# Kernel optimization log

Measured on AMD Instinct MI355X. Metric: run time of the kernel, lower is better.

Reference implementation:

```python
import jax, jax.numpy as jnp
import numpy as np

N = 100000   # nodes
E = 1600000  # edges
F_IN = 256   # nfeat
H = 64       # hidden_sizes
C = 40       # nclass


def gcn_norm(edge_index, edge_weight, num_nodes):
    # Add self-loops with weight 1 (PyG gcn_norm default fill_value=1.0)
    loop = jnp.arange(num_nodes)
    row = jnp.concatenate([edge_index[0], loop])
    col = jnp.concatenate([edge_index[1], loop])
    w = jnp.concatenate([edge_weight, jnp.ones((num_nodes,), edge_weight.dtype)])
    # Symmetric normalization: D^-1/2 A D^-1/2 (degree computed at target, per PyG)
    deg = jax.ops.segment_sum(w, col, num_segments=num_nodes)
    deg_inv_sqrt = jnp.where(deg > 0, jax.lax.rsqrt(deg), 0.0)
    norm = deg_inv_sqrt[row] * w * deg_inv_sqrt[col]
    return row, col, norm


def gcn_conv(x, W, b, row, col, norm, num_nodes):
    # Linear transform first (shrinks feature dim before irregular traffic)
    x = x @ W                                    # [N, out]
    msgs = norm[:, None] * x[row]                # gather + scale: [E+N, out]
    out = jax.ops.segment_sum(msgs, col, num_segments=num_nodes)  # scatter-add
    return out + b


def setup_inputs() -> dict:
    key = jax.random.key(0)
    k = jax.random.split(key, 7)
    x = jax.random.normal(k[0], (N, F_IN), dtype=jnp.float32)
    edge_index = jax.random.randint(k[1], (2, E), 0, N, dtype=jnp.int64)
    edge_attr = jax.random.uniform(k[2], (E,), dtype=jnp.float32)
    W1 = jax.random.normal(k[3], (F_IN, H), dtype=jnp.float32) * (1.0 / np.sqrt(F_IN))
    b1 = jnp.zeros((H,), jnp.float32)
    W2 = jax.random.normal(k[4], (H, C), dtype=jnp.float32) * (1.0 / np.sqrt(H))
    b2 = jnp.zeros((C,), jnp.float32)
    return {"x": x, "edge_index": edge_index, "edge_attr": edge_attr,
            "W1": W1, "b1": b1, "W2": W2, "b2": b2}


def reference(x, edge_index, edge_attr, W1, b1, W2, b2):
    row, col, norm = gcn_norm(edge_index, edge_attr, N)
    h = jax.nn.relu(gcn_conv(x, W1, b1, row, col, norm, N))
    # F.dropout with training=False is identity (eval mode)
    final = gcn_conv(h, W2, b2, row, col, norm, N)
    return final, jax.nn.log_softmax(final, axis=1)
```

## Files before the change

### kernel.cpp

```cpp
#include <hip/hip_runtime.h>
#include <hip/hip_bf16.h>
#include <math.h>

#define NN 100000
#define EE 1600000
#define FIN 256
#define HID 64
#define NC 40
#define NB 196
#define BCAP 10240
#define CHUNK 2048
#define NBKB ((EE + CHUNK - 1) / CHUNK)

typedef unsigned long long ull;
typedef __attribute__((ext_vector_type(8))) short short8;
typedef __attribute__((ext_vector_type(4))) float f32x4;

__device__ __forceinline__ unsigned short f2bf_rne(float f) {
    unsigned u = __float_as_uint(f);
    u += 0x7FFFu + ((u >> 16) & 1u);
    return (unsigned short)(u >> 16);
}
__device__ __forceinline__ float bf2f(unsigned short b) {
    return __uint_as_float((unsigned)b << 16);
}

__global__ __launch_bounds__(256) void bucket_kernel(const int* __restrict__ row,
                                                     const int* __restrict__ col,
                                                     const float* __restrict__ w,
                                                     int* __restrict__ bucket_cnt,
                                                     int2* __restrict__ staging) {
    __shared__ int2 spay[CHUNK];
    __shared__ int2 sorted[CHUNK];
    __shared__ unsigned char sb[CHUNK];
    __shared__ unsigned char sbk[CHUNK];
    __shared__ int lcnt[NB], lofs[NB], lstart[NB];
    __shared__ int sscan[256];
    const int tid = threadIdx.x;
    const int e0 = blockIdx.x * CHUNK;
    const int nE = min(CHUNK, EE - e0);
    for (int i = tid; i < nE; i += 256) {
        int e = e0 + i;
        int c = col[e];
        sb[i] = (unsigned char)(c >> 9);
        spay[i] = make_int2(((c & 511) << 17) | row[e], __float_as_int(w[e]));
    }
    for (int i = tid; i < NB; i += 256) lcnt[i] = 0;
    __syncthreads();
    for (int i = tid; i < nE; i += 256) atomicAdd(&lcnt[sb[i]], 1);
    __syncthreads();
    int v = (tid < NB) ? lcnt[tid] : 0;
    sscan[tid] = v;
    __syncthreads();
    for (int off = 1; off < 256; off <<= 1) {
        int u = (tid >= off) ? sscan[tid - off] : 0;
        __syncthreads();
        sscan[tid] += u;
        __syncthreads();
    }
    if (tid < NB) {
        lofs[tid] = sscan[tid] - v;
        lstart[tid] = v ? atomicAdd(&bucket_cnt[tid], v) : 0;
        lcnt[tid] = 0;
    }
    __syncthreads();
    for (int i = tid; i < nE; i += 256) {
        int b = sb[i];
        int p = lofs[b] + atomicAdd(&lcnt[b], 1);
        sorted[p] = spay[i];
        sbk[p] = (unsigned char)b;
    }
    __syncthreads();
    for (int p = tid; p < nE; p += 256) {
        int b = sbk[p];
        int slot = lstart[b] + (p - lofs[b]);
        if (slot < BCAP) staging[(size_t)b * BCAP + slot] = sorted[p];
    }
}

__global__ __launch_bounds__(256) void bscan_w1cvt_kernel(int* __restrict__ bucket_cnt,
                                                          int* __restrict__ bucket_base,
                                                          const float* __restrict__ W1,
                                                          unsigned short* __restrict__ w1hi,
                                                          unsigned short* __restrict__ w1lo) {
    if (blockIdx.x == 0) {
        __shared__ int sd[256];
        int t = threadIdx.x;
        int v = (t < NB) ? min(bucket_cnt[t], BCAP) : 0;
        sd[t] = v;
        __syncthreads();
        for (int off = 1; off < 256; off <<= 1) {
            int u = (t >= off) ? sd[t - off] : 0;
            __syncthreads();
            sd[t] += u;
            __syncthreads();
        }
        if (t < NB) { bucket_base[t] = sd[t] - v; bucket_cnt[t] = v; }
    } else {
        int b = blockIdx.x - 1;
        for (int i = threadIdx.x; i < 4096; i += 256) {
            int e = b * 4096 + i;
            int c = e >> 8, k = e & 255;
            float v = W1[(size_t)k * HID + c];
            unsigned short h = f2bf_rne(v);
            w1hi[e] = h;
            w1lo[e] = f2bf_rne(v - bf2f(h));
        }
    }
}

__global__ __launch_bounds__(512) void build_count_kernel(const int2* __restrict__ staging,
                                                          const int* __restrict__ bucket_cnt,
                                                          const int* __restrict__ bucket_base,
                                                          int* __restrict__ basev,
                                                          int* __restrict__ endv,
                                                          float* __restrict__ dis) {
    __shared__ int dcnt[512];
    __shared__ float dsum[512];
    __shared__ int sscan[512];
    const int t = threadIdx.x;
    const int b = blockIdx.x;
    const int nE = bucket_cnt[b];
    const int ebase = bucket_base[b];
    const int2* st = staging + (size_t)b * BCAP;
    dcnt[t] = 0; dsum[t] = 0.f;
    __syncthreads();
    for (int i = t; i < nE; i += 512) {
        int2 p = st[i];
        int d = p.x >> 17;
        atomicAdd(&dcnt[d], 1);
        atomicAdd(&dsum[d], __int_as_float(p.y));
    }
    __syncthreads();
    int c = dcnt[t];
    sscan[t] = c;
    __syncthreads();
    for (int off = 1; off < 512; off <<= 1) {
        int u = (t >= off) ? sscan[t - off] : 0;
        __syncthreads();
        sscan[t] += u;
        __syncthreads();
    }
    int gb = ebase + sscan[t] - c;
    int gd = b * 512 + t;
    if (gd < NN) {
        basev[gd] = gb;
        endv[gd] = gb + c;
        dis[gd] = rsqrtf(dsum[t] + 1.0f);
    }
}

__global__ __launch_bounds__(512) void build_place_kernel(const int2* __restrict__ staging,
                                                          const int* __restrict__ bucket_cnt,
                                                          const int* __restrict__ basev,
                                                          const float* __restrict__ dis,
                                                          int2* __restrict__ eme) {
    __shared__ int dcur[512];
    __shared__ float sdis[512];
    const int t = threadIdx.x;
    const int b = blockIdx.x;
    const int nE = bucket_cnt[b];
    const int2* st = staging + (size_t)b * BCAP;
    const int gd = b * 512 + t;
    dcur[t] = (gd < NN) ? basev[gd] : 0;
    sdis[t] = (gd < NN) ? dis[gd] : 0.f;
    __syncthreads();
    for (int i = t; i < nE; i += 512) {
        int2 p = st[i];
        int d = p.x >> 17;
        int src = p.x & 0x1FFFF;
        int pos = atomicAdd(&dcur[d], 1);
        float wn = __int_as_float(p.y) * dis[src] * sdis[d];
        eme[pos] = make_int2(src, __float_as_int(wn));
    }
}

__global__ __launch_bounds__(256) void gemm1_mfma_kernel(const float* __restrict__ x,
                                                         const unsigned short* __restrict__ w1hi,
                                                         const unsigned short* __restrict__ w1lo,
                                                         __hip_bfloat16* __restrict__ xw) {
    const int tid = threadIdx.x;
    const int wid = tid >> 6;
    const int l   = tid & 63;
    const int r   = l & 15;
    const int kg  = l >> 4;
    const int rb0 = blockIdx.x * 128 + wid * 32;

    f32x4 acc[2][4];
#pragma unroll
    for (int i = 0; i < 2; i++)
#pragma unroll
        for (int j = 0; j < 4; j++) acc[i][j] = (f32x4){0.f, 0.f, 0.f, 0.f};

    int row0 = rb0 + r;
    int row1 = rb0 + 16 + r;
    int row0c = row0 < NN ? row0 : NN - 1;
    int row1c = row1 < NN ? row1 : NN - 1;
    const float* a0p = x + (size_t)row0c * FIN + kg * 8;
    const float* a1p = x + (size_t)row1c * FIN + kg * 8;

#pragma unroll
    for (int ks = 0; ks < 8; ks++) {
        short8 bhi[4], blo[4];
#pragma unroll
        for (int ct = 0; ct < 4; ct++) {
            size_t off = (size_t)(ct * 16 + r) * FIN + ks * 32 + kg * 8;
            bhi[ct] = *(const short8*)(w1hi + off);
            blo[ct] = *(const short8*)(w1lo + off);
        }
        float4 af0a = *(const float4*)(a0p + ks * 32);
        float4 af0b = *(const float4*)(a0p + ks * 32 + 4);
        float4 af1a = *(const float4*)(a1p + ks * 32);
        float4 af1b = *(const float4*)(a1p + ks * 32 + 4);
        float a0v[8] = {af0a.x, af0a.y, af0a.z, af0a.w, af0b.x, af0b.y, af0b.z, af0b.w};
        float a1v[8] = {af1a.x, af1a.y, af1a.z, af1a.w, af1b.x, af1b.y, af1b.z, af1b.w};
        short8 ahi0, alo0, ahi1, alo1;
#pragma unroll
        for (int j = 0; j < 8; j++) {
            unsigned short h0 = f2bf_rne(a0v[j]);
            ahi0[j] = (short)h0;
            alo0[j] = (short)f2bf_rne(a0v[j] - bf2f(h0));
            unsigned short h1 = f2bf_rne(a1v[j]);
            ahi1[j] = (short)h1;
            alo1[j] = (short)f2bf_rne(a1v[j] - bf2f(h1));
        }
#pragma unroll
        for (int ct = 0; ct < 4; ct++) {
            acc[0][ct] = __builtin_amdgcn_mfma_f32_16x16x32_bf16(ahi0, bhi[ct], acc[0][ct], 0, 0, 0);
            acc[0][ct] = __builtin_amdgcn_mfma_f32_16x16x32_bf16(ahi0, blo[ct], acc[0][ct], 0, 0, 0);
            acc[0][ct] = __builtin_amdgcn_mfma_f32_16x16x32_bf16(alo0, bhi[ct], acc[0][ct], 0, 0, 0);
            acc[1][ct] = __builtin_amdgcn_mfma_f32_16x16x32_bf16(ahi1, bhi[ct], acc[1][ct], 0, 0, 0);
            acc[1][ct] = __builtin_amdgcn_mfma_f32_16x16x32_bf16(ahi1, blo[ct], acc[1][ct], 0, 0, 0);
            acc[1][ct] = __builtin_amdgcn_mfma_f32_16x16x32_bf16(alo1, bhi[ct], acc[1][ct], 0, 0, 0);
        }
    }
#pragma unroll
    for (int rt = 0; rt < 2; rt++) {
#pragma unroll
        for (int i = 0; i < 4; i++) {
            int grow = rb0 + rt * 16 + kg * 4 + i;
            if (grow < NN) {
                unsigned short* dst = (unsigned short*)xw + (size_t)grow * HID + r;
#pragma unroll
                for (int ct = 0; ct < 4; ct++)
                    dst[ct * 16] = f2bf_rne(acc[rt][ct][i]);
            }
        }
    }
}

__global__ __launch_bounds__(256) void gather1_kernel(const int* __restrict__ basev,
                                                      const int* __restrict__ endv,
                                                      const ull* __restrict__ eme,
                                                      const unsigned* __restrict__ xw32,
                                                      const float* __restrict__ dis,
                                                      const float* __restrict__ b,
                                                      float* __restrict__ h) {
    int n = blockIdx.x * 4 + (threadIdx.x >> 6);
    if (n >= NN) return;
    int lane = threadIdx.x & 63;
    int half = lane >> 5;
    int fl = lane & 31;
    int s = basev[n], t = endv[n];
    int deg = t - s;
    float acc0 = 0.f, acc1 = 0.f;
    int nbt = (deg + 15) >> 4;
    for (int bi = 0; bi < nbt; bi++) {
        int p0 = s + bi * 16 + half;
        ull q[8];
#pragma unroll
        for (int j = 0; j < 8; j++) {
            int idx = p0 + 2 * j;
            int c = idx < t ? idx : (t - 1);
            q[j] = __builtin_nontemporal_load(&eme[c]);
        }
        unsigned u[8];
        float wv[8];
#pragma unroll
        for (int j = 0; j < 8; j++) {
            unsigned src = (unsigned)q[j] & 0x1FFFFu;
            u[j] = xw32[(src << 5) | fl];
            wv[j] = (p0 + 2 * j < t) ? __int_as_float((int)(q[j] >> 32)) : 0.f;
        }
#pragma unroll
        for (int j = 0; j < 8; j++) {
            acc0 += wv[j] * __uint_as_float(u[j] << 16);
            acc1 += wv[j] * __uint_as_float(u[j] & 0xFFFF0000u);
        }
    }
    acc0 += __shfl_xor(acc0, 32);
    acc1 += __shfl_xor(acc1, 32);
    float d = dis[n];
    unsigned un = xw32[((unsigned)n << 5) | fl];
    float2 bv = *(const float2*)(b + 2 * fl);
    float v0 = acc0 + d * d * __uint_as_float(un << 16) + bv.x;
    float v1 = acc1 + d * d * __uint_as_float(un & 0xFFFF0000u) + bv.y;
    if (lane < 32) {
        *(float2*)(h + (size_t)n * HID + 2 * fl) = make_float2(fmaxf(v0, 0.f), fmaxf(v1, 0.f));
    }
}

__global__ __launch_bounds__(256) void gemm2_kernel(const float* __restrict__ h,
                                                    const float* __restrict__ W,
                                                    __hip_bfloat16* __restrict__ hw) {
    __shared__ float hs[64][65];
    __shared__ float Ws[HID * NC];
    const int tid = threadIdx.x;
    const int base = blockIdx.x * 64;
    for (int v = tid; v < 1024; v += 256) {
        int r = v >> 4, q = v & 15;
        int gr = base + r;
        float4 hv = make_float4(0.f, 0.f, 0.f, 0.f);
        if (gr < NN) hv = *(const float4*)(h + (size_t)gr * HID + q * 4);
        hs[r][q * 4 + 0] = hv.x; hs[r][q * 4 + 1] = hv.y;
        hs[r][q * 4 + 2] = hv.z; hs[r][q * 4 + 3] = hv.w;
    }
    for (int v = tid; v < HID * NC; v += 256) Ws[v] = W[v];
    __syncthreads();
    const int tx = tid & 7;
    const int ty = tid >> 3;
    float acc[2][5] = {};
#pragma unroll 8
    for (int k = 0; k < HID; k++) {
        float h0 = hs[ty * 2 + 0][k];
        float h1 = hs[ty * 2 + 1][k];
        const float* wr = &Ws[k * NC + tx * 5];
        float w0 = wr[0], w1 = wr[1], w2 = wr[2], w3 = wr[3], w4 = wr[4];
        acc[0][0] += h0 * w0; acc[0][1] += h0 * w1; acc[0][2] += h0 * w2;
        acc[0][3] += h0 * w3; acc[0][4] += h0 * w4;
        acc[1][0] += h1 * w0; acc[1][1] += h1 * w1; acc[1][2] += h1 * w2;
        acc[1][3] += h1 * w3; acc[1][4] += h1 * w4;
    }
#pragma unroll
    for (int i = 0; i < 2; i++) {
        int gr = base + ty * 2 + i;
        if (gr < NN) {
#pragma unroll
            for (int c = 0; c < 5; c++)
                hw[(size_t)gr * 64 + tx * 5 + c] = __float2bfloat16(acc[i][c]);
        }
    }
}

__global__ __launch_bounds__(256) void gather2_kernel(const int* __restrict__ basev,
                                                      const int* __restrict__ endv,
                                                      const ull* __restrict__ eme,
                                                      const unsigned* __restrict__ hw32,
                                                      const float* __restrict__ dis,
                                                      const float* __restrict__ b,
                                                      float* __restrict__ out) {
    int n = blockIdx.x * 4 + (threadIdx.x >> 6);
    if (n >= NN) return;
    int lane = threadIdx.x & 63;
    int half = lane >> 5;
    int fl = lane & 31;
    bool act = fl < 20;
    int s = basev[n], t = endv[n];
    int deg = t - s;
    float acc0 = 0.f, acc1 = 0.f;
    int nbt = (deg + 15) >> 4;
    for (int bi = 0; bi < nbt; bi++) {
        int p0 = s + bi * 16 + half;
        ull q[8];
#pragma unroll
        for (int j = 0; j < 8; j++) {
            int idx = p0 + 2 * j;
            int c = idx < t ? idx : (t - 1);
            q[j] = __builtin_nontemporal_load(&eme[c]);
        }
        unsigned u[8];
        float wv[8];
#pragma unroll
        for (int j = 0; j < 8; j++) {
            unsigned src = (unsigned)q[j] & 0x1FFFFu;
            u[j] = hw32[(src << 5) | fl];
            wv[j] = (p0 + 2 * j < t) ? __int_as_float((int)(q[j] >> 32)) : 0.f;
        }
#pragma unroll
        for (int j = 0; j < 8; j++) {
            acc0 += wv[j] * __uint_as_float(u[j] << 16);
            acc1 += wv[j] * __uint_as_float(u[j] & 0xFFFF0000u);
        }
    }
    acc0 += __shfl_xor(acc0, 32);
    acc1 += __shfl_xor(acc1, 32);
    float v0 = 0.f, v1 = 0.f, m = -INFINITY;
    if (act) {
        float d = dis[n];
        unsigned un = hw32[((unsigned)n << 5) | fl];
        float2 bv = *(const float2*)(b + 2 * fl);
        v0 = acc0 + d * d * __uint_as_float(un << 16) + bv.x;
        v1 = acc1 + d * d * __uint_as_float(un & 0xFFFF0000u) + bv.y;
        m = fmaxf(v0, v1);
    }
#pragma unroll
    for (int off = 16; off; off >>= 1) m = fmaxf(m, __shfl_xor(m, off));
    float e0 = act ? expf(v0 - m) : 0.f;
    float e1 = act ? expf(v1 - m) : 0.f;
    float sum = e0 + e1;
#pragma unroll
    for (int off = 16; off; off >>= 1) sum += __shfl_xor(sum, off);
    float lse = m + logf(sum);
    if (act && lane < 32) {
        size_t idx = (size_t)n * NC + 2 * fl;
        *(float2*)(out + idx) = make_float2(v0, v1);
        *(float2*)(out + (size_t)NN * NC + idx) = make_float2(v0 - lse, v1 - lse);
    }
}

extern "C" void kernel_launch(void* const* d_in, const int* in_sizes, int n_in,
                              void* d_out, int out_size, void* d_ws, size_t ws_size,
                              hipStream_t stream) {
    const float* x    = (const float*)d_in[0];
    const int*   eidx = (const int*)d_in[1];
    const float* ew   = (const float*)d_in[2];
    const float* W1   = (const float*)d_in[3];
    const float* b1   = (const float*)d_in[4];
    const float* W2   = (const float*)d_in[5];
    const float* b2   = (const float*)d_in[6];
    float* out = (float*)d_out;

    const int* row = eidx;
    const int* col = eidx + EE;

    char* ws = (char*)d_ws;
    int*   bucket_cnt  = (int*)ws;               ws += 256 * 4;
    int*   bucket_base = (int*)ws;               ws += 256 * 4;
    float* dis    = (float*)ws;                  ws += NN * 4;
    int*   basev  = (int*)ws;                    ws += NN * 4;
    int*   endv   = (int*)ws;                    ws += NN * 4;
    int2*  eme    = (int2*)ws;                   ws += (size_t)EE * 8;
    __hip_bfloat16* xw = (__hip_bfloat16*)ws;    ws += (size_t)NN * HID * 2;
    char* unionp = ws;                           ws += (size_t)NN * HID * 4;
    int2*  staging = (int2*)unionp;
    float* h       = (float*)unionp;
    __hip_bfloat16* hw2 = (__hip_bfloat16*)ws;   ws += (size_t)NN * 64 * 2;
    unsigned short* w1hi = (unsigned short*)ws;  ws += (size_t)HID * FIN * 2;
    unsigned short* w1lo = (unsigned short*)ws;  ws += (size_t)HID * FIN * 2;

    hipMemsetAsync(bucket_cnt, 0, 256 * 4, stream);

    bucket_kernel<<<NBKB, 256, 0, stream>>>(row, col, ew, bucket_cnt, staging);
    bscan_w1cvt_kernel<<<5, 256, 0, stream>>>(bucket_cnt, bucket_base, W1, w1hi, w1lo);
    build_count_kernel<<<NB, 512, 0, stream>>>(staging, bucket_cnt, bucket_base,
                                               basev, endv, dis);
    build_place_kernel<<<NB, 512, 0, stream>>>(staging, bucket_cnt, basev, dis, eme);
    gemm1_mfma_kernel<<<(NN + 127) / 128, 256, 0, stream>>>(x, w1hi, w1lo, xw);
    gather1_kernel<<<(NN + 3) / 4, 256, 0, stream>>>(basev, endv, (const ull*)eme,
                                                     (const unsigned*)xw, dis, b1, h);
    gemm2_kernel<<<(NN + 63) / 64, 256, 0, stream>>>(h, W2, hw2);
    gather2_kernel<<<(NN + 3) / 4, 256, 0, stream>>>(basev, endv, (const ull*)eme,
                                                     (const unsigned*)hw2, dis, b2, out);
}
```

Before: 411.9 us.

## Pad per-node edge lists to multiples of 8 for vectorized branch-free gathers

The CSR build now pads each destination node's edge segment to a multiple of 8 with zero-weight entries. Because of this, the build kernels are reordered: counts and padded per-bucket totals come first, then the bucket scan, then placement plus the pad fill. Both gather kernels then read edges with 16-byte vector loads and no per-edge bounds clamping or masking. The cost is more edge storage and extra wasted gather work on padding entries, which all read row 0 of the feature table. The nontemporal load hint is also dropped.

```diff
diff --git a/kernel.cpp b/kernel.cpp
--- a/kernel.cpp
+++ b/kernel.cpp
@@ -13,6 +13,7 @@
 #define NBKB ((EE + CHUNK - 1) / CHUNK)
 
 typedef unsigned long long ull;
+typedef __attribute__((ext_vector_type(2))) unsigned long long ullx2;
 typedef __attribute__((ext_vector_type(8))) short short8;
 typedef __attribute__((ext_vector_type(4))) float f32x4;
 
@@ -23,6 +24,15 @@
 }
 __device__ __forceinline__ float bf2f(unsigned short b) {
     return __uint_as_float((unsigned)b << 16);
+}
+
+__device__ __forceinline__ void edge_acc(ull q, const unsigned* __restrict__ tbl,
+                                         int fl, float& a0, float& a1) {
+    unsigned src = (unsigned)q & 0x1FFFFu;
+    unsigned u = tbl[(src << 5) | fl];
+    float w = __int_as_float((int)(q >> 32));
+    a0 += w * __uint_as_float(u << 16);
+    a1 += w * __uint_as_float(u & 0xFFFF0000u);
 }
 
 __global__ __launch_bounds__(256) void bucket_kernel(const int* __restrict__ row,
@@ -78,7 +88,48 @@
     }
 }
 
-__global__ __launch_bounds__(256) void bscan_w1cvt_kernel(int* __restrict__ bucket_cnt,
+__global__ __launch_bounds__(512) void build_count_kernel(const int2* __restrict__ staging,
+                                                          const int* __restrict__ bucket_cnt,
+                                                          int* __restrict__ basev,
+                                                          int* __restrict__ endv,
+                                                          float* __restrict__ dis,
+                                                          int* __restrict__ ptot) {
+    __shared__ int dcnt[512];
+    __shared__ float dsum[512];
+    __shared__ int sscan[512];
+    const int t = threadIdx.x;
+    const int b = blockIdx.x;
+    const int nE = min(bucket_cnt[b], BCAP);
+    const int2* st = staging + (size_t)b * BCAP;
+    dcnt[t] = 0; dsum[t] = 0.f;
+    __syncthreads();
+    for (int i = t; i < nE; i += 512) {
+        int2 p = st[i];
+        int d = p.x >> 17;
+        atomicAdd(&dcnt[d], 1);
+        atomicAdd(&dsum[d], __int_as_float(p.y));
+    }
+    __syncthreads();
+    int c = dcnt[t];
+    int pdeg = (c + 7) & ~7;
+    sscan[t] = pdeg;
+    __syncthreads();
+    for (int off = 1; off < 512; off <<= 1) {
+        int u = (t >= off) ? sscan[t - off] : 0;
+        __syncthreads();
+        sscan[t] += u;
+        __syncthreads();
+    }
+    int gd = b * 512 + t;
+    if (gd < NN) {
+        basev[gd] = sscan[t] - pdeg;
+        endv[gd] = c;
+        dis[gd] = rsqrtf(dsum[t] + 1.0f);
+    }
+    if (t == 511) ptot[b] = sscan[511];
+}
+
+__global__ __launch_bounds__(256) void bscan_w1cvt_kernel(const int* __restrict__ ptot,
                                                           int* __restrict__ bucket_base,
                                                           const float* __restrict__ W1,
                                                           unsigned short* __restrict__ w1hi,
@@ -86,7 +137,7 @@
     if (blockIdx.x == 0) {
         __shared__ int sd[256];
         int t = threadIdx.x;
-        int v = (t < NB) ? min(bucket_cnt[t], BCAP) : 0;
+        int v = (t < NB) ? ptot[t] : 0;
         sd[t] = v;
         __syncthreads();
         for (int off = 1; off < 256; off <<= 1) {
@@ -95,7 +146,7 @@
             sd[t] += u;
             __syncthreads();
         }
-        if (t < NB) { bucket_base[t] = sd[t] - v; bucket_cnt[t] = v; }
+        if (t < NB) bucket_base[t] = sd[t] - v;
     } else {
         int b = blockIdx.x - 1;
         for (int i = threadIdx.x; i < 4096; i += 256) {
@@ -109,61 +160,32 @@
     }
 }
 
-__global__ __launch_bounds__(512) void build_count_kernel(const int2* __restrict__ staging,
+__global__ __launch_bounds__(512) void build_place_kernel(const int2* __restrict__ staging,
                                                           const int* __restrict__ bucket_cnt,
                                                           const int* __restrict__ bucket_base,
                                                           int* __restrict__ basev,
                                                           int* __restrict__ endv,
-                                                          float* __restrict__ dis) {
-    __shared__ int dcnt[512];
-    __shared__ float dsum[512];
-    __shared__ int sscan[512];
-    const int t = threadIdx.x;
-    const int b = blockIdx.x;
-    const int nE = bucket_cnt[b];
-    const int ebase = bucket_base[b];
-    const int2* st = staging + (size_t)b * BCAP;
-    dcnt[t] = 0; dsum[t] = 0.f;
-    __syncthreads();
-    for (int i = t; i < nE; i += 512) {
-        int2 p = st[i];
-        int d = p.x >> 17;
-        atomicAdd(&dcnt[d], 1);
-        atomicAdd(&dsum[d], __int_as_float(p.y));
-    }
-    __syncthreads();
-    int c = dcnt[t];
-    sscan[t] = c;
-    __syncthreads();
-    for (int off = 1; off < 512; off <<= 1) {
-        int u = (t >= off) ? sscan[t - off] : 0;
-        __syncthreads();
-        sscan[t] += u;
-        __syncthreads();
-    }
-    int gb = ebase + sscan[t] - c;
-    int gd = b * 512 + t;
-    if (gd < NN) {
-        basev[gd] = gb;
-        endv[gd] = gb + c;
-        dis[gd] = rsqrtf(dsum[t] + 1.0f);
-    }
-}
-
-__global__ __launch_bounds__(512) void build_place_kernel(const int2* __restrict__ staging,
-                                                          const int* __restrict__ bucket_cnt,
-                                                          const int* __restrict__ basev,
                                                           const float* __restrict__ dis,
                                                           int2* __restrict__ eme) {
     __shared__ int dcur[512];
     __shared__ float sdis[512];
     const int t = threadIdx.x;
     const int b = blockIdx.x;
-    const int nE = bucket_cnt[b];
+    const int nE = min(bucket_cnt[b], BCAP);
     const int2* st = staging + (size_t)b * BCAP;
     const int gd = b * 512 + t;
-    dcur[t] = (gd < NN) ? basev[gd] : 0;
-    sdis[t] = (gd < NN) ? dis[gd] : 0.f;
+    int gb = 0, c = 0, pdeg = 0;
+    if (gd < NN) {
+        gb = bucket_base[b] + basev[gd];
+        c = endv[gd];
+        pdeg = (c + 7) & ~7;
+        basev[gd] = gb;
+        endv[gd] = gb + c;
+        sdis[t] = dis[gd];
+    } else {
+        sdis[t] = 0.f;
+    }
+    dcur[t] = gb;
     __syncthreads();
     for (int i = t; i < nE; i += 512) {
         int2 p = st[i];
@@ -173,6 +195,7 @@
         float wn = __int_as_float(p.y) * dis[src] * sdis[d];
         eme[pos] = make_int2(src, __float_as_int(wn));
     }
+    for (int i = c; i < pdeg; i++) eme[gb + i] = make_int2(0, 0);
 }
 
 __global__ __launch_bounds__(256) void gemm1_mfma_kernel(const float* __restrict__ x,
@@ -262,31 +285,32 @@
     int half = lane >> 5;
     int fl = lane & 31;
     int s = basev[n], t = endv[n];
-    int deg = t - s;
+    int pdeg = (t - s + 7) & ~7;
     float acc0 = 0.f, acc1 = 0.f;
-    int nbt = (deg + 15) >> 4;
-    for (int bi = 0; bi < nbt; bi++) {
-        int p0 = s + bi * 16 + half;
-        ull q[8];
-#pragma unroll
-        for (int j = 0; j < 8; j++) {
-            int idx = p0 + 2 * j;
-            int c = idx < t ? idx : (t - 1);
-            q[j] = __builtin_nontemporal_load(&eme[c]);
-        }
-        unsigned u[8];
-        float wv[8];
-#pragma unroll
-        for (int j = 0; j < 8; j++) {
-            unsigned src = (unsigned)q[j] & 0x1FFFFu;
-            u[j] = xw32[(src << 5) | fl];
-            wv[j] = (p0 + 2 * j < t) ? __int_as_float((int)(q[j] >> 32)) : 0.f;
-        }
-#pragma unroll
-        for (int j = 0; j < 8; j++) {
-            acc0 += wv[j] * __uint_as_float(u[j] << 16);
-            acc1 += wv[j] * __uint_as_float(u[j] & 0xFFFF0000u);
-        }
+    int nb16 = pdeg >> 4;
+    for (int bi = 0; bi < nb16; bi++) {
+        const ull* pp = eme + s + bi * 16 + 8 * half;
+        ullx2 qa = *(const ullx2*)(pp);
+        ullx2 qb = *(const ullx2*)(pp + 2);
+        ullx2 qc = *(const ullx2*)(pp + 4);
+        ullx2 qd = *(const ullx2*)(pp + 6);
+        edge_acc(qa[0], xw32, fl, acc0, acc1);
+        edge_acc(qa[1], xw32, fl, acc0, acc1);
+        edge_acc(qb[0], xw32, fl, acc0, acc1);
+        edge_acc(qb[1], xw32, fl, acc0, acc1);
+        edge_acc(qc[0], xw32, fl, acc0, acc1);
+        edge_acc(qc[1], xw32, fl, acc0, acc1);
+        edge_acc(qd[0], xw32, fl, acc0, acc1);
+        edge_acc(qd[1], xw32, fl, acc0, acc1);
+    }
+    if (pdeg & 8) {
+        const ull* pp = eme + s + nb16 * 16 + 4 * half;
+        ullx2 qa = *(const ullx2*)(pp);
+        ullx2 qb = *(const ullx2*)(pp + 2);
+        edge_acc(qa[0], xw32, fl, acc0, acc1);
+        edge_acc(qa[1], xw32, fl, acc0, acc1);
+        edge_acc(qb[0], xw32, fl, acc0, acc1);
+        edge_acc(qb[1], xw32, fl, acc0, acc1);
     }
     acc0 += __shfl_xor(acc0, 32);
     acc1 += __shfl_xor(acc1, 32);
@@ -356,31 +380,32 @@
     int fl = lane & 31;
     bool act = fl < 20;
     int s = basev[n], t = endv[n];
-    int deg = t - s;
+    int pdeg = (t - s + 7) & ~7;
     float acc0 = 0.f, acc1 = 0.f;
-    int nbt = (deg + 15) >> 4;
-    for (int bi = 0; bi < nbt; bi++) {
-        int p0 = s + bi * 16 + half;
-        ull q[8];
-#pragma unroll
-        for (int j = 0; j < 8; j++) {
-            int idx = p0 + 2 * j;
-            int c = idx < t ? idx : (t - 1);
-            q[j] = __builtin_nontemporal_load(&eme[c]);
-        }
-        unsigned u[8];
-        float wv[8];
-#pragma unroll
-        for (int j = 0; j < 8; j++) {
-            unsigned src = (unsigned)q[j] & 0x1FFFFu;
-            u[j] = hw32[(src << 5) | fl];
-            wv[j] = (p0 + 2 * j < t) ? __int_as_float((int)(q[j] >> 32)) : 0.f;
-        }
-#pragma unroll
-        for (int j = 0; j < 8; j++) {
-            acc0 += wv[j] * __uint_as_float(u[j] << 16);
-            acc1 += wv[j] * __uint_as_float(u[j] & 0xFFFF0000u);
-        }
+    int nb16 = pdeg >> 4;
+    for (int bi = 0; bi < nb16; bi++) {
+        const ull* pp = eme + s + bi * 16 + 8 * half;
+        ullx2 qa = *(const ullx2*)(pp);
+        ullx2 qb = *(const ullx2*)(pp + 2);
+        ullx2 qc = *(const ullx2*)(pp + 4);
+        ullx2 qd = *(const ullx2*)(pp + 6);
+        edge_acc(qa[0], hw32, fl, acc0, acc1);
+        edge_acc(qa[1], hw32, fl, acc0, acc1);
+        edge_acc(qb[0], hw32, fl, acc0, acc1);
+        edge_acc(qb[1], hw32, fl, acc0, acc1);
+        edge_acc(qc[0], hw32, fl, acc0, acc1);
+        edge_acc(qc[1], hw32, fl, acc0, acc1);
+        edge_acc(qd[0], hw32, fl, acc0, acc1);
+        edge_acc(qd[1], hw32, fl, acc0, acc1);
+    }
+    if (pdeg & 8) {
+        const ull* pp = eme + s + nb16 * 16 + 4 * half;
+        ullx2 qa = *(const ullx2*)(pp);
+        ullx2 qb = *(const ullx2*)(pp + 2);
+        edge_acc(qa[0], hw32, fl, acc0, acc1);
+        edge_acc(qa[1], hw32, fl, acc0, acc1);
+        edge_acc(qb[0], hw32, fl, acc0, acc1);
+        edge_acc(qb[1], hw32, fl, acc0, acc1);
     }
     acc0 += __shfl_xor(acc0, 32);
     acc1 += __shfl_xor(acc1, 32);
@@ -426,10 +451,11 @@
     char* ws = (char*)d_ws;
     int*   bucket_cnt  = (int*)ws;               ws += 256 * 4;
     int*   bucket_base = (int*)ws;               ws += 256 * 4;
+    int*   ptot        = (int*)ws;               ws += 256 * 4;
     float* dis    = (float*)ws;                  ws += NN * 4;
     int*   basev  = (int*)ws;                    ws += NN * 4;
     int*   endv   = (int*)ws;                    ws += NN * 4;
-    int2*  eme    = (int2*)ws;                   ws += (size_t)EE * 8;
+    int2*  eme    = (int2*)ws;                   ws += ((size_t)EE + 8 * NN) * 8;
     __hip_bfloat16* xw = (__hip_bfloat16*)ws;    ws += (size_t)NN * HID * 2;
     char* unionp = ws;                           ws += (size_t)NN * HID * 4;
     int2*  staging = (int2*)unionp;
@@ -441,10 +467,11 @@
     hipMemsetAsync(bucket_cnt, 0, 256 * 4, stream);
 
     bucket_kernel<<<NBKB, 256, 0, stream>>>(row, col, ew, bucket_cnt, staging);
-    bscan_w1cvt_kernel<<<5, 256, 0, stream>>>(bucket_cnt, bucket_base, W1, w1hi, w1lo);
-    build_count_kernel<<<NB, 512, 0, stream>>>(staging, bucket_cnt, bucket_base,
-                                               basev, endv, dis);
-    build_place_kernel<<<NB, 512, 0, stream>>>(staging, bucket_cnt, basev, dis, eme);
+    build_count_kernel<<<NB, 512, 0, stream>>>(staging, bucket_cnt,
+                                               basev, endv, dis, ptot);
+    bscan_w1cvt_kernel<<<5, 256, 0, stream>>>(ptot, bucket_base, W1, w1hi, w1lo);
+    build_place_kernel<<<NB, 512, 0, stream>>>(staging, bucket_cnt, bucket_base,
+                                               basev, endv, dis, eme);
     gemm1_mfma_kernel<<<(NN + 127) / 128, 256, 0, stream>>>(x, w1hi, w1lo, xw);
     gather1_kernel<<<(NN + 3) / 4, 256, 0, stream>>>(basev, endv, (const ull*)eme,
                                                      (const unsigned*)xw, dis, b1, h);
```

Result: faster. 370.5 us (-10.0%).
